# Performance work log

Hardware: AMD Instinct MI355X
Metric: run time of the kernel (lower is better)

Reference implementation:

```python
import jax, jax.numpy as jnp
import numpy as np

DIM = 512
HEADS = 8
DHEAD = DIM // 8          # 64
INNER = HEADS * DHEAD     # 512
M_LANDMARKS = 256
PINV_ITERS = 6
KSZ = 33                  # residual depthwise conv kernel (default)


def setup_inputs() -> dict:
    key = jax.random.key(0)
    ks = jax.random.split(key, 5)
    B, N = 1, 16384
    s = DIM ** -0.5
    return {
        "x": jax.random.normal(ks[0], (B, N, DIM), jnp.float32),
        "norm_w": jnp.ones((DIM,), jnp.float32),
        "norm_b": jnp.zeros((DIM,), jnp.float32),
        "w_qkv": jax.random.normal(ks[1], (3 * INNER, DIM), jnp.float32) * s,   # Linear(dim, 3*inner, bias=False)
        "w_out": jax.random.normal(ks[2], (DIM, INNER), jnp.float32) * s,        # Linear(inner, dim)
        "b_out": jnp.zeros((DIM,), jnp.float32),
        "conv_w": jax.random.normal(ks[3], (HEADS, 1, KSZ, 1), jnp.float32) * 0.1,  # depthwise Conv2d(h,h,(33,1),groups=h)
    }


def _layernorm(x, w, b, eps=1e-5):
    mu = x.mean(-1, keepdims=True)
    var = ((x - mu) ** 2).mean(-1, keepdims=True)
    return (x - mu) * jax.lax.rsqrt(var + eps) * w + b


def _moore_penrose_pinv(a, iters):
    # a: [B, H, m, m]; matches lucidrains moore_penrose_iter_pinv (global max over col/row sums)
    abs_a = jnp.abs(a)
    col = abs_a.sum(-1).max()
    row = abs_a.sum(-2).max()
    z = jnp.swapaxes(a, -1, -2) / (col * row)
    I = jnp.eye(a.shape[-1], dtype=a.dtype)
    for _ in range(iters):
        az = a @ z
        z = 0.25 * z @ (13 * I - az @ (15 * I - az @ (7 * I - az)))
    return z


def _nystrom_attention(h, w_qkv, w_out, b_out, conv_w):
    B, N, _ = h.shape
    qkv = h @ w_qkv.T                          # [B, N, 3*inner]
    q, k, v = jnp.split(qkv, 3, axis=-1)

    def heads(t):
        return t.reshape(B, N, HEADS, DHEAD).transpose(0, 2, 1, 3)  # [B, H, N, d]
    q = heads(q) * (DHEAD ** -0.5)
    k = heads(k)
    v = heads(v)

    # landmark pooling: mean over contiguous groups of size l = N / m
    l = N // M_LANDMARKS
    q_l = q.reshape(B, HEADS, M_LANDMARKS, l, DHEAD).mean(3)   # [B, H, m, d]
    k_l = k.reshape(B, HEADS, M_LANDMARKS, l, DHEAD).mean(3)

    attn1 = jax.nn.softmax(jnp.einsum('bhnd,bhmd->bhnm', q, k_l), axis=-1)      # [B,H,N,m]
    attn2 = jax.nn.softmax(jnp.einsum('bhid,bhjd->bhij', q_l, k_l), axis=-1)    # [B,H,m,m]
    attn3 = jax.nn.softmax(jnp.einsum('bhmd,bhnd->bhmn', q_l, k), axis=-1)      # [B,H,m,N]

    attn2_inv = _moore_penrose_pinv(attn2, PINV_ITERS)
    out = attn1 @ (attn2_inv @ (attn3 @ v))                                     # [B,H,N,d]

    # residual depthwise conv along sequence dim (kernel 33x1, groups=HEADS, no bias)
    conv = jax.lax.conv_general_dilated(
        v, conv_w, window_strides=(1, 1),
        padding=((KSZ // 2, KSZ // 2), (0, 0)),
        dimension_numbers=('NCHW', 'OIHW', 'NCHW'),
        feature_group_count=HEADS)
    out = out + conv

    out = out.transpose(0, 2, 1, 3).reshape(B, N, INNER)
    return out @ w_out.T + b_out


def reference(x, norm_w, norm_b, w_qkv, w_out, b_out, conv_w):
    h = _layernorm(x, norm_w, norm_b)
    return x + _nystrom_attention(h, w_qkv, w_out, b_out, conv_w)
```

## Files before the change

### kernel.cpp

```cpp
#include <hip/hip_runtime.h>
#include <hip/hip_bf16.h>


typedef __attribute__((ext_vector_type(8))) short bf16x8;
typedef __attribute__((ext_vector_type(4))) float f32x4;

#define MFMA16(A, B, C) __builtin_amdgcn_mfma_f32_16x16x32_bf16(A, B, C, 0, 0, 0)
#define GLD16(g, l) __builtin_amdgcn_global_load_lds( \
    (const __attribute__((address_space(1))) void*)(g), \
    (__attribute__((address_space(3))) void*)(l), 16, 0, 0)

static __device__ __forceinline__ unsigned short f2b(float f) {
  __hip_bfloat16 h = __float2bfloat16(f);
  return *reinterpret_cast<unsigned short*>(&h);
}
static __device__ __forceinline__ float b2f(unsigned short u) {
  return __uint_as_float(((unsigned)u) << 16);
}

#define FMA16(ACC, AV, BV) do { \
  ACC[0][0] += AV.x*BV.x; ACC[0][1] += AV.x*BV.y; ACC[0][2] += AV.x*BV.z; ACC[0][3] += AV.x*BV.w; \
  ACC[1][0] += AV.y*BV.x; ACC[1][1] += AV.y*BV.y; ACC[1][2] += AV.y*BV.z; ACC[1][3] += AV.y*BV.w; \
  ACC[2][0] += AV.z*BV.x; ACC[2][1] += AV.z*BV.y; ACC[2][2] += AV.z*BV.z; ACC[2][3] += AV.z*BV.w; \
  ACC[3][0] += AV.w*BV.x; ACC[3][1] += AV.w*BV.y; ACC[3][2] += AV.w*BV.z; ACC[3][3] += AV.w*BV.w; \
} while (0)

__global__ __launch_bounds__(128) void k_ln(const float* __restrict__ x,
    const float* __restrict__ w, const float* __restrict__ b, unsigned short* __restrict__ h) {
  const int row = blockIdx.x;
  const int t = threadIdx.x;
  const float4 xv = ((const float4*)(x + (size_t)row * 512))[t];
  float s  = xv.x + xv.y + xv.z + xv.w;
  float sq = xv.x*xv.x + xv.y*xv.y + xv.z*xv.z + xv.w*xv.w;
  #pragma unroll
  for (int o = 32; o > 0; o >>= 1) {
    s  += __shfl_down(s, o, 64);
    sq += __shfl_down(sq, o, 64);
  }
  __shared__ float ls[2], lq[2];
  if ((t & 63) == 0) { ls[t >> 6] = s; lq[t >> 6] = sq; }
  __syncthreads();
  s = ls[0] + ls[1]; sq = lq[0] + lq[1];
  const float mean = s * (1.0f / 512.0f);
  const float var  = sq * (1.0f / 512.0f) - mean * mean;
  const float rstd = rsqrtf(var + 1e-5f);
  const float4 wv = ((const float4*)w)[t];
  const float4 bv = ((const float4*)b)[t];
  ushort4 hv;
  hv.x = f2b((xv.x - mean) * rstd * wv.x + bv.x);
  hv.y = f2b((xv.y - mean) * rstd * wv.y + bv.y);
  hv.z = f2b((xv.z - mean) * rstd * wv.z + bv.z);
  hv.w = f2b((xv.w - mean) * rstd * wv.w + bv.w);
  ((ushort4*)(h + (size_t)row * 512))[t] = hv;
}

__global__ __launch_bounds__(256) void k_cvt(const float* __restrict__ src,
    unsigned short* __restrict__ dst, int n4) {
  const int i = blockIdx.x * 256 + threadIdx.x;
  if (i < n4) {
    const float4 f = ((const float4*)src)[i];
    ushort4 u;
    u.x = f2b(f.x); u.y = f2b(f.y); u.z = f2b(f.z); u.w = f2b(f.w);
    ((ushort4*)dst)[i] = u;
  }
}

__global__ __launch_bounds__(256) void k_qkv_mfma(const unsigned short* __restrict__ A,
    const unsigned short* __restrict__ B,
    unsigned short* __restrict__ qb, unsigned short* __restrict__ kb,
    unsigned short* __restrict__ vb) {
  __shared__ unsigned short As[128 * 32];
  __shared__ unsigned short Bs[128 * 32];
  const int t = threadIdx.x;
  const int lane = t & 63, w = t >> 6;
  const int quad = lane >> 4, l15 = lane & 15;
  const int wm = (w >> 1) * 64, wn = (w & 1) * 64;
  const int m0 = blockIdx.y * 128, n0 = blockIdx.x * 128;
  f32x4 acc[4][4];
  #pragma unroll
  for (int i = 0; i < 4; ++i)
    #pragma unroll
    for (int j = 0; j < 4; ++j) acc[i][j] = (f32x4){0.f, 0.f, 0.f, 0.f};
  for (int k0 = 0; k0 < 512; k0 += 32) {
    __syncthreads();
    #pragma unroll
    for (int c = 0; c < 2; ++c) {
      const int slot = c * 256 + t;
      const int row = slot >> 2, seg = slot & 3;
      GLD16(A + (size_t)(m0 + row) * 512 + k0 + seg * 8, As + slot * 8);
      GLD16(B + (size_t)(n0 + row) * 512 + k0 + seg * 8, Bs + slot * 8);
    }
    __syncthreads();
    bf16x8 a[4], b[4];
    #pragma unroll
    for (int i = 0; i < 4; ++i)
      a[i] = *(const bf16x8*)(As + (wm + i * 16 + l15) * 32 + quad * 8);
    #pragma unroll
    for (int j = 0; j < 4; ++j)
      b[j] = *(const bf16x8*)(Bs + (wn + j * 16 + l15) * 32 + quad * 8);
    #pragma unroll
    for (int i = 0; i < 4; ++i)
      #pragma unroll
      for (int j = 0; j < 4; ++j)
        acc[i][j] = MFMA16(a[i], b[j], acc[i][j]);
  }
  const int part = n0 >> 9;
  #pragma unroll
  for (int i = 0; i < 4; ++i)
    #pragma unroll
    for (int j = 0; j < 4; ++j)
      #pragma unroll
      for (int r = 0; r < 4; ++r) {
        const int row = m0 + wm + i * 16 + quad * 4 + r;
        const int col = n0 + wn + j * 16 + l15;
        const int rem = col & 511;
        const int hd = rem >> 6, dd = rem & 63;
        const size_t idx = ((size_t)hd * 16384 + row) * 64 + dd;
        const float val = acc[i][j][r];
        if (part == 0)      qb[idx] = f2b(val * 0.125f);
        else if (part == 1) kb[idx] = f2b(val);
        else                vb[idx] = f2b(val);
      }
}

__global__ __launch_bounds__(256) void k_tr(const unsigned short* __restrict__ v,
    unsigned short* __restrict__ vt) {
  __shared__ unsigned short T[64][72];
  const int t = threadIdx.x;
  const int n0 = blockIdx.x * 64, h = blockIdx.y;
  const int n = t >> 2, sg = (t & 3) * 16;
  const unsigned short* p = v + ((size_t)(h * 16384 + n0 + n)) * 64 + sg;
  #pragma unroll
  for (int i = 0; i < 16; i += 4) {
    const ushort4 u = *(const ushort4*)(p + i);
    T[sg + i + 0][n] = u.x; T[sg + i + 1][n] = u.y;
    T[sg + i + 2][n] = u.z; T[sg + i + 3][n] = u.w;
  }
  __syncthreads();
  const int d = t >> 2, so = (t & 3) * 16;
  unsigned short* q = vt + ((size_t)(h * 64 + d)) * 16384 + n0 + so;
  #pragma unroll
  for (int i = 0; i < 16; i += 4) {
    ushort4 u;
    u.x = T[d][so + i]; u.y = T[d][so + i + 1];
    u.z = T[d][so + i + 2]; u.w = T[d][so + i + 3];
    *(ushort4*)(q + i) = u;
  }
}

__global__ __launch_bounds__(256) void k_landmark(const unsigned short* __restrict__ qb,
    const unsigned short* __restrict__ kb, float* __restrict__ qlf,
    unsigned short* __restrict__ qlb, float* __restrict__ klf,
    unsigned short* __restrict__ klb) {
  const int t = threadIdx.x, d = t & 63, grp = t >> 6;
  const int m = blockIdx.x, h = blockIdx.y;
  const unsigned short* src = blockIdx.z ? kb : qb;
  const unsigned short* p = src + ((size_t)h * 16384 + m * 64 + grp * 16) * 64 + d;
  float s = 0.f;
  #pragma unroll
  for (int i = 0; i < 16; ++i) s += b2f(p[(size_t)i * 64]);
  __shared__ float red[4][64];
  red[grp][d] = s;
  __syncthreads();
  if (t < 64) {
    float v = (red[0][d] + red[1][d]) + (red[2][d] + red[3][d]);
    v *= (1.0f / 64.0f);
    const size_t oi = ((size_t)h * 256 + m) * 64 + d;
    if (blockIdx.z == 0) { qlf[oi] = v; qlb[oi] = f2b(v); }
    else                 { klf[oi] = v; klb[oi] = f2b(v); }
  }
}

__global__ __launch_bounds__(256) void k_attn2(const float* __restrict__ ql,
    const float* __restrict__ kl, float* __restrict__ a2, unsigned short* __restrict__ a2b) {
  const int i = blockIdx.x, h = blockIdx.y, j = threadIdx.x;
  __shared__ float qrow[64];
  __shared__ float wred[4];
  __shared__ float wsum[4];
  if (j < 64) qrow[j] = ql[((size_t)h * 256 + i) * 64 + j];
  __syncthreads();
  const float* kr = kl + ((size_t)h * 256 + j) * 64;
  float s = 0.f;
  #pragma unroll 8
  for (int d = 0; d < 64; ++d) s += qrow[d] * kr[d];
  float mx = s;
  #pragma unroll
  for (int o2 = 32; o2 > 0; o2 >>= 1) mx = fmaxf(mx, __shfl_xor(mx, o2, 64));
  if ((j & 63) == 0) wred[j >> 6] = mx;
  __syncthreads();
  mx = fmaxf(fmaxf(wred[0], wred[1]), fmaxf(wred[2], wred[3]));
  const float e = __expf(s - mx);
  float sm = e;
  #pragma unroll
  for (int o2 = 32; o2 > 0; o2 >>= 1) sm += __shfl_xor(sm, o2, 64);
  if ((j & 63) == 0) wsum[j >> 6] = sm;
  __syncthreads();
  sm = wsum[0] + wsum[1] + wsum[2] + wsum[3];
  const float v = e / sm;
  const size_t idx = ((size_t)h * 256 + i) * 256 + j;
  a2[idx] = v;
  a2b[idx] = f2b(v);
}

__global__ __launch_bounds__(256) void k_colsum(const float* __restrict__ a2,
    float* __restrict__ cm) {
  const int h = blockIdx.x, j = threadIdx.x;
  const float* p = a2 + (size_t)h * 65536 + j;
  float s = 0.f;
  for (int i = 0; i < 256; ++i) s += p[(size_t)i * 256];
  float mx = s;
  #pragma unroll
  for (int o2 = 32; o2 > 0; o2 >>= 1) mx = fmaxf(mx, __shfl_xor(mx, o2, 64));
  __shared__ float wred[4];
  if ((j & 63) == 0) wred[j >> 6] = mx;
  __syncthreads();
  if (j == 0) cm[h] = fmaxf(fmaxf(wred[0], wred[1]), fmaxf(wred[2], wred[3]));
}

__global__ __launch_bounds__(256) void k_z0(const float* __restrict__ a2,
    const float* __restrict__ cm, unsigned short* __restrict__ z0b,
    unsigned short* __restrict__ z0t) {
  __shared__ float T[64][65];
  const int bi = blockIdx.x, bj = blockIdx.y, h = blockIdx.z;
  const int t = threadIdx.x;
  const int r = t >> 2, cseg = (t & 3) * 16;
  float g = cm[0];
  #pragma unroll
  for (int c = 1; c < 8; ++c) g = fmaxf(g, cm[c]);
  const float inv = 1.0f / g;
  const float* p = a2 + ((size_t)h * 256 + bj * 64 + r) * 256 + bi * 64 + cseg;
  unsigned short* qt = z0t + ((size_t)h * 256 + bj * 64 + r) * 256 + bi * 64 + cseg;
  #pragma unroll
  for (int i = 0; i < 16; i += 4) {
    const float4 f = *(const float4*)(p + i);
    T[cseg + i + 0][r] = f.x; T[cseg + i + 1][r] = f.y;
    T[cseg + i + 2][r] = f.z; T[cseg + i + 3][r] = f.w;
    ushort4 u;
    u.x = f2b(f.x * inv); u.y = f2b(f.y * inv);
    u.z = f2b(f.z * inv); u.w = f2b(f.w * inv);
    *(ushort4*)(qt + i) = u;
  }
  __syncthreads();
  unsigned short* qb_ = z0b + ((size_t)h * 256 + bi * 64 + r) * 256 + bj * 64 + cseg;
  #pragma unroll
  for (int i = 0; i < 16; i += 4) {
    ushort4 u;
    u.x = f2b(T[r][cseg + i] * inv);     u.y = f2b(T[r][cseg + i + 1] * inv);
    u.z = f2b(T[r][cseg + i + 2] * inv); u.w = f2b(T[r][cseg + i + 3] * inv);
    *(ushort4*)(qb_ + i) = u;
  }
}

__global__ __launch_bounds__(256) void k_pgemm(const unsigned short* __restrict__ A,
    const unsigned short* __restrict__ Bt, unsigned short* __restrict__ Cn,
    unsigned short* __restrict__ Ct, float* __restrict__ Cf,
    float alpha, float sdiag, int use_diag) {
  __shared__ unsigned short As[64 * 128];
  __shared__ unsigned short Bs[64 * 128];
  const int t = threadIdx.x;
  const int lane = t & 63, w = t >> 6;
  const int quad = lane >> 4, l15 = lane & 15;
  const int bn = blockIdx.x, bm = blockIdx.y, h = blockIdx.z;
  const size_t hs = (size_t)h * 65536;
  const unsigned short* Ap = A + hs + (size_t)(bm * 64) * 256;
  const unsigned short* Bp = Bt + hs + (size_t)(bn * 64) * 256;
  f32x4 acc[4];
  #pragma unroll
  for (int j = 0; j < 4; ++j) acc[j] = (f32x4){0.f, 0.f, 0.f, 0.f};
  for (int kh = 0; kh < 2; ++kh) {
    __syncthreads();
    #pragma unroll
    for (int c = 0; c < 4; ++c) {
      const int slot = c * 256 + t;
      const int row = slot >> 4, pc = slot & 15;
      const int lc = pc ^ (row & 7);
      GLD16(Ap + (size_t)row * 256 + kh * 128 + lc * 8, As + slot * 8);
      GLD16(Bp + (size_t)row * 256 + kh * 128 + lc * 8, Bs + slot * 8);
    }
    __syncthreads();
    #pragma unroll
    for (int kc = 0; kc < 4; ++kc) {
      const int arow = w * 16 + l15;
      const bf16x8 a = *(const bf16x8*)(As + arow * 128 + ((kc * 4 + quad) ^ (arow & 7)) * 8);
      #pragma unroll
      for (int j = 0; j < 4; ++j) {
        const int brow = j * 16 + l15;
        const bf16x8 b = *(const bf16x8*)(Bs + brow * 128 + ((kc * 4 + quad) ^ (brow & 7)) * 8);
        acc[j] = MFMA16(a, b, acc[j]);
      }
    }
  }
  const int row0 = bm * 64 + w * 16 + quad * 4;
  #pragma unroll
  for (int j = 0; j < 4; ++j) {
    const int col = bn * 64 + j * 16 + l15;
    float v[4];
    #pragma unroll
    for (int r = 0; r < 4; ++r) v[r] = acc[j][r] * alpha;
    if (Cn) {
      #pragma unroll
      for (int r = 0; r < 4; ++r) Cn[hs + (size_t)(row0 + r) * 256 + col] = f2b(v[r]);
    }
    if (Cf) {
      #pragma unroll
      for (int r = 0; r < 4; ++r) Cf[hs + (size_t)(row0 + r) * 256 + col] = v[r];
    }
    ushort4 u;
    float tv[4];
    #pragma unroll
    for (int r = 0; r < 4; ++r)
      tv[r] = use_diag ? ((col == row0 + r ? sdiag : 0.f) - v[r]) : v[r];
    u.x = f2b(tv[0]); u.y = f2b(tv[1]); u.z = f2b(tv[2]); u.w = f2b(tv[3]);
    *(ushort4*)(Ct + hs + (size_t)col * 256 + row0) = u;
  }
}

__global__ __launch_bounds__(256) void k_gemm256(const float* __restrict__ A,
    const float* __restrict__ B, float* __restrict__ C,
    int lda, int ldb, int ldc,
    unsigned long long sA, unsigned long long sB, unsigned long long sC,
    float alpha, float sdiag, int use_diag,
    const float* __restrict__ rs, unsigned long long sRS) {
  A += (size_t)blockIdx.z * sA;
  B += (size_t)blockIdx.z * sB;
  C += (size_t)blockIdx.z * sC;
  if (rs) rs += (size_t)blockIdx.z * sRS;
  __shared__ float As[16][68];
  __shared__ float Bs[16][68];
  const int t = threadIdx.x, tx = t & 15, ty = t >> 4;
  const int bn = blockIdx.x, bm = blockIdx.y;
  const int lr = t >> 2, lk = (t & 3) << 2;
  const int bkr = t >> 4, bnc = (t & 15) << 2;
  float acc[4][4] = {{0.f}};
  for (int k0 = 0; k0 < 256; k0 += 16) {
    float4 a4 = *(const float4*)(A + (size_t)(bm * 64 + lr) * lda + k0 + lk);
    float4 b4 = *(const float4*)(B + (size_t)(k0 + bkr) * ldb + bn * 64 + bnc);
    if (use_diag) {
      const int kg = k0 + bkr, ngb = bn * 64 + bnc;
      b4.x = (kg == ngb + 0 ? sdiag : 0.f) - b4.x;
      b4.y = (kg == ngb + 1 ? sdiag : 0.f) - b4.y;
      b4.z = (kg == ngb + 2 ? sdiag : 0.f) - b4.z;
      b4.w = (kg == ngb + 3 ? sdiag : 0.f) - b4.w;
    }
    if (rs) {
      const float rv = 1.0f / rs[k0 + bkr];
      b4.x *= rv; b4.y *= rv; b4.z *= rv; b4.w *= rv;
    }
    __syncthreads();
    As[lk+0][lr] = a4.x; As[lk+1][lr] = a4.y; As[lk+2][lr] = a4.z; As[lk+3][lr] = a4.w;
    *(float4*)&Bs[bkr][bnc] = b4;
    __syncthreads();
    #pragma unroll
    for (int kq = 0; kq < 16; ++kq) {
      const float4 av = *(const float4*)&As[kq][ty << 2];
      const float4 bv = *(const float4*)&Bs[kq][tx << 2];
      FMA16(acc, av, bv);
    }
  }
  #pragma unroll
  for (int ii = 0; ii < 4; ++ii)
    #pragma unroll
    for (int jj = 0; jj < 4; ++jj)
      C[(size_t)(bm * 64 + (ty << 2) + ii) * ldc + bn * 64 + (tx << 2) + jj] =
          alpha * acc[ii][jj];
}

__global__ __launch_bounds__(256) void k_trD(const float* __restrict__ D,
    unsigned short* __restrict__ dt) {
  __shared__ float T[64][65];
  const int t = threadIdx.x;
  const int mc = blockIdx.x, h = blockIdx.y;
  const int m = t >> 2, sg = (t & 3) * 16;
  const float* p = D + ((size_t)(h * 256 + mc * 64 + m)) * 64 + sg;
  #pragma unroll
  for (int i = 0; i < 16; i += 4) {
    const float4 f = *(const float4*)(p + i);
    T[sg + i + 0][m] = f.x; T[sg + i + 1][m] = f.y;
    T[sg + i + 2][m] = f.z; T[sg + i + 3][m] = f.w;
  }
  __syncthreads();
  const int d = t >> 2, so = (t & 3) * 16;
  unsigned short* q = dt + ((size_t)(h * 64 + d)) * 256 + mc * 64 + so;
  #pragma unroll
  for (int i = 0; i < 16; i += 4) {
    ushort4 u;
    u.x = f2b(T[d][so + i]);     u.y = f2b(T[d][so + i + 1]);
    u.z = f2b(T[d][so + i + 2]); u.w = f2b(T[d][so + i + 3]);
    *(ushort4*)(q + i) = u;
  }
}

__global__ __launch_bounds__(256) void k_w3_mfma(const unsigned short* __restrict__ qlb,
    const unsigned short* __restrict__ kb, const unsigned short* __restrict__ vt,
    float* __restrict__ W, float* __restrict__ lsum) {
  __shared__ unsigned short QLs[64 * 64];
  __shared__ unsigned short Ks [64 * 64];
  __shared__ unsigned short Vts[64 * 64];
  __shared__ unsigned short Ps [64 * 64];
  const int t = threadIdx.x;
  const int lane = t & 63, w = t >> 6;
  const int quad = lane >> 4, l15 = lane & 15;
  const int kc = blockIdx.x, mt = blockIdx.y, h = blockIdx.z;
  #pragma unroll
  for (int c = 0; c < 2; ++c) {
    const int slot = c * 256 + t;
    const int row = slot >> 3, pc = slot & 7, lc = pc ^ (row & 7);
    GLD16(qlb + ((size_t)(h * 256 + mt * 64 + row)) * 64 + lc * 8, QLs + slot * 8);
  }
  __syncthreads();
  const int arow = w * 16 + l15;
  const bf16x8 aq0 = *(const bf16x8*)(QLs + arow * 64 + ((quad    ) ^ (arow & 7)) * 8);
  const bf16x8 aq1 = *(const bf16x8*)(QLs + arow * 64 + ((quad + 4) ^ (arow & 7)) * 8);
  f32x4 wacc[4];
  #pragma unroll
  for (int dt = 0; dt < 4; ++dt) wacc[dt] = (f32x4){0.f, 0.f, 0.f, 0.f};
  float lacc[4] = {0.f, 0.f, 0.f, 0.f};
  for (int ss = 0; ss < 16; ++ss) {
    const int n0 = kc * 1024 + ss * 64;
    __syncthreads();
    #pragma unroll
    for (int c = 0; c < 2; ++c) {
      const int slot = c * 256 + t;
      const int row = slot >> 3, pc = slot & 7, lc = pc ^ (row & 7);
      GLD16(kb + ((size_t)(h * 16384 + n0 + row)) * 64 + lc * 8, Ks + slot * 8);
      GLD16(vt + ((size_t)(h * 64 + row)) * 16384 + n0 + lc * 8, Vts + slot * 8);
    }
    __syncthreads();
    f32x4 s[4];
    #pragma unroll
    for (int j = 0; j < 4; ++j) {
      s[j] = (f32x4){0.f, 0.f, 0.f, 0.f};
      const int brow = j * 16 + l15;
      const bf16x8 b0 = *(const bf16x8*)(Ks + brow * 64 + ((quad    ) ^ (brow & 7)) * 8);
      const bf16x8 b1 = *(const bf16x8*)(Ks + brow * 64 + ((quad + 4) ^ (brow & 7)) * 8);
      s[j] = MFMA16(aq0, b0, s[j]);
      s[j] = MFMA16(aq1, b1, s[j]);
    }
    #pragma unroll
    for (int j = 0; j < 4; ++j)
      #pragma unroll
      for (int r = 0; r < 4; ++r) {
        const float e = __expf(s[j][r]);
        lacc[r] += e;
        const int prow = w * 16 + quad * 4 + r, pcol = j * 16 + l15;
        Ps[prow * 64 + (((pcol >> 3) ^ (prow & 7)) << 3) + (pcol & 7)] = f2b(e);
      }
    __syncthreads();
    const bf16x8 ap0 = *(const bf16x8*)(Ps + arow * 64 + ((quad    ) ^ (arow & 7)) * 8);
    const bf16x8 ap1 = *(const bf16x8*)(Ps + arow * 64 + ((quad + 4) ^ (arow & 7)) * 8);
    #pragma unroll
    for (int dt = 0; dt < 4; ++dt) {
      const int brow = dt * 16 + l15;
      const bf16x8 b0 = *(const bf16x8*)(Vts + brow * 64 + ((quad    ) ^ (brow & 7)) * 8);
      const bf16x8 b1 = *(const bf16x8*)(Vts + brow * 64 + ((quad + 4) ^ (brow & 7)) * 8);
      wacc[dt] = MFMA16(ap0, b0, wacc[dt]);
      wacc[dt] = MFMA16(ap1, b1, wacc[dt]);
    }
  }
  #pragma unroll
  for (int dt = 0; dt < 4; ++dt)
    #pragma unroll
    for (int r = 0; r < 4; ++r)
      atomicAdd(&W[((size_t)(h * 256 + mt * 64 + w * 16 + quad * 4 + r)) * 64 + dt * 16 + l15],
                wacc[dt][r]);
  #pragma unroll
  for (int r = 0; r < 4; ++r) {
    #pragma unroll
    for (int msk = 1; msk < 16; msk <<= 1) lacc[r] += __shfl_xor(lacc[r], msk, 64);
    if (l15 == 0)
      atomicAdd(&lsum[h * 256 + mt * 64 + w * 16 + quad * 4 + r], lacc[r]);
  }
}

__global__ __launch_bounds__(256) void k_attn1_mfma(const unsigned short* __restrict__ qb,
    const unsigned short* __restrict__ klb, const unsigned short* __restrict__ dtb,
    const unsigned short* __restrict__ vt, const float* __restrict__ cw,
    unsigned short* __restrict__ o) {
  __shared__ unsigned short Wb[64 * 96];
  __shared__ unsigned short Ks[64 * 64];
  __shared__ unsigned short Ds[64 * 64];
  __shared__ unsigned short Ps[64 * 64];
  __shared__ float Wsm[33];
  const int t = threadIdx.x;
  const int lane = t & 63, w = t >> 6;
  const int quad = lane >> 4, l15 = lane & 15;
  const int bt = blockIdx.x, h = blockIdx.y;
  const int n0 = bt * 64;
  if (t < 33) Wsm[t] = cw[h * 33 + t];
  #pragma unroll
  for (int c = 0; c < 2; ++c) {
    const int slot = c * 256 + t;
    const int row = slot >> 3, pc = slot & 7, lc = pc ^ (row & 7);
    GLD16(qb + ((size_t)(h * 16384 + n0 + row)) * 64 + lc * 8, Wb + slot * 8);
  }
  __syncthreads();
  const int arow = w * 16 + l15;
  const bf16x8 aq0 = *(const bf16x8*)(Wb + arow * 64 + ((quad    ) ^ (arow & 7)) * 8);
  const bf16x8 aq1 = *(const bf16x8*)(Wb + arow * 64 + ((quad + 4) ^ (arow & 7)) * 8);
  __syncthreads();
  {
    const int n = t >> 2;
    const int gb = (t & 3) * 24;
    #pragma unroll
    for (int i = 0; i < 24; ++i) {
      const int g = gb + i;
      const int j = g - n;
      const int src = n0 - 16 + g;
      const float val = (j >= 0 && j <= 32 && src >= 0 && src < 16384) ? Wsm[j] : 0.f;
      Wb[n * 96 + (((g >> 3) ^ (n & 3)) << 3) + (g & 7)] = f2b(val);
    }
  }
  __syncthreads();
  f32x4 cacc[4];
  #pragma unroll
  for (int dt = 0; dt < 4; ++dt) cacc[dt] = (f32x4){0.f, 0.f, 0.f, 0.f};
  #pragma unroll
  for (int kcc = 0; kcc < 3; ++kcc) {
    const bf16x8 a = *(const bf16x8*)(Wb + arow * 96 + (((kcc * 4 + quad) ^ (arow & 3)) << 3));
    int off = n0 - 16 + kcc * 32 + quad * 8;
    off = off < 0 ? 0 : (off > 16376 ? 16376 : off);
    #pragma unroll
    for (int dt = 0; dt < 4; ++dt) {
      const bf16x8 b = *(const bf16x8*)(vt + ((size_t)(h * 64 + dt * 16 + l15)) * 16384 + off);
      cacc[dt] = MFMA16(a, b, cacc[dt]);
    }
  }
  f32x4 oacc[4];
  #pragma unroll
  for (int dt = 0; dt < 4; ++dt) oacc[dt] = (f32x4){0.f, 0.f, 0.f, 0.f};
  float lacc[4] = {0.f, 0.f, 0.f, 0.f};
  for (int mc = 0; mc < 4; ++mc) {
    const int m0 = mc * 64;
    __syncthreads();
    #pragma unroll
    for (int c = 0; c < 2; ++c) {
      const int slot = c * 256 + t;
      const int row = slot >> 3, pc = slot & 7, lc = pc ^ (row & 7);
      GLD16(klb + ((size_t)(h * 256 + m0 + row)) * 64 + lc * 8, Ks + slot * 8);
      GLD16(dtb + ((size_t)(h * 64 + row)) * 256 + m0 + lc * 8, Ds + slot * 8);
    }
    __syncthreads();
    f32x4 s[4];
    #pragma unroll
    for (int j = 0; j < 4; ++j) {
      s[j] = (f32x4){0.f, 0.f, 0.f, 0.f};
      const int brow = j * 16 + l15;
      const bf16x8 b0 = *(const bf16x8*)(Ks + brow * 64 + ((quad    ) ^ (brow & 7)) * 8);
      const bf16x8 b1 = *(const bf16x8*)(Ks + brow * 64 + ((quad + 4) ^ (brow & 7)) * 8);
      s[j] = MFMA16(aq0, b0, s[j]);
      s[j] = MFMA16(aq1, b1, s[j]);
    }
    #pragma unroll
    for (int j = 0; j < 4; ++j)
      #pragma unroll
      for (int r = 0; r < 4; ++r) {
        const float e = __expf(s[j][r]);
        lacc[r] += e;
        const int prow = w * 16 + quad * 4 + r, pcol = j * 16 + l15;
        Ps[prow * 64 + (((pcol >> 3) ^ (prow & 7)) << 3) + (pcol & 7)] = f2b(e);
      }
    __syncthreads();
    const bf16x8 ap0 = *(const bf16x8*)(Ps + arow * 64 + ((quad    ) ^ (arow & 7)) * 8);
    const bf16x8 ap1 = *(const bf16x8*)(Ps + arow * 64 + ((quad + 4) ^ (arow & 7)) * 8);
    #pragma unroll
    for (int dt = 0; dt < 4; ++dt) {
      const int brow = dt * 16 + l15;
      const bf16x8 b0 = *(const bf16x8*)(Ds + brow * 64 + ((quad    ) ^ (brow & 7)) * 8);
      const bf16x8 b1 = *(const bf16x8*)(Ds + brow * 64 + ((quad + 4) ^ (brow & 7)) * 8);
      oacc[dt] = MFMA16(ap0, b0, oacc[dt]);
      oacc[dt] = MFMA16(ap1, b1, oacc[dt]);
    }
  }
  #pragma unroll
  for (int r = 0; r < 4; ++r)
    #pragma unroll
    for (int msk = 1; msk < 16; msk <<= 1) lacc[r] += __shfl_xor(lacc[r], msk, 64);
  #pragma unroll
  for (int dt = 0; dt < 4; ++dt)
    #pragma unroll
    for (int r = 0; r < 4; ++r) {
      const float val = oacc[dt][r] / lacc[r] + cacc[dt][r];
      o[((size_t)(n0 + w * 16 + quad * 4 + r)) * 512 + h * 64 + dt * 16 + l15] = f2b(val);
    }
}

__global__ __launch_bounds__(256) void k_out_mfma(const unsigned short* __restrict__ A,
    const unsigned short* __restrict__ B, const float* __restrict__ bias,
    const float* __restrict__ xres, float* __restrict__ out) {
  __shared__ unsigned short As[128 * 32];
  __shared__ unsigned short Bs[128 * 32];
  const int t = threadIdx.x;
  const int lane = t & 63, w = t >> 6;
  const int quad = lane >> 4, l15 = lane & 15;
  const int wm = (w >> 1) * 64, wn = (w & 1) * 64;
  const int m0 = blockIdx.y * 128, n0 = blockIdx.x * 128;
  f32x4 acc[4][4];
  #pragma unroll
  for (int i = 0; i < 4; ++i)
    #pragma unroll
    for (int j = 0; j < 4; ++j) acc[i][j] = (f32x4){0.f, 0.f, 0.f, 0.f};
  for (int k0 = 0; k0 < 512; k0 += 32) {
    __syncthreads();
    #pragma unroll
    for (int c = 0; c < 2; ++c) {
      const int slot = c * 256 + t;
      const int row = slot >> 2, seg = slot & 3;
      GLD16(A + (size_t)(m0 + row) * 512 + k0 + seg * 8, As + slot * 8);
      GLD16(B + (size_t)(n0 + row) * 512 + k0 + seg * 8, Bs + slot * 8);
    }
    __syncthreads();
    bf16x8 a[4], b[4];
    #pragma unroll
    for (int i = 0; i < 4; ++i)
      a[i] = *(const bf16x8*)(As + (wm + i * 16 + l15) * 32 + quad * 8);
    #pragma unroll
    for (int j = 0; j < 4; ++j)
      b[j] = *(const bf16x8*)(Bs + (wn + j * 16 + l15) * 32 + quad * 8);
    #pragma unroll
    for (int i = 0; i < 4; ++i)
      #pragma unroll
      for (int j = 0; j < 4; ++j)
        acc[i][j] = MFMA16(a[i], b[j], acc[i][j]);
  }
  #pragma unroll
  for (int i = 0; i < 4; ++i)
    #pragma unroll
    for (int j = 0; j < 4; ++j)
      #pragma unroll
      for (int r = 0; r < 4; ++r) {
        const int row = m0 + wm + i * 16 + quad * 4 + r;
        const int col = n0 + wn + j * 16 + l15;
        out[(size_t)row * 512 + col] = acc[i][j][r] + bias[col] + xres[(size_t)row * 512 + col];
      }
}

extern "C" void kernel_launch(void* const* d_in, const int* in_sizes, int n_in,
                              void* d_out, int out_size, void* d_ws, size_t ws_size,
                              hipStream_t stream) {
  const float* x      = (const float*)d_in[0];
  const float* norm_w = (const float*)d_in[1];
  const float* norm_b = (const float*)d_in[2];
  const float* w_qkv  = (const float*)d_in[3];
  const float* w_out  = (const float*)d_in[4];
  const float* b_out  = (const float*)d_in[5];
  const float* conv_w = (const float*)d_in[6];
  float* out = (float*)d_out;

  char* cur = (char*)d_ws;
  auto alloc = [&](size_t bytes) -> char* {
    char* p = cur;
    cur += (bytes + 255) & ~(size_t)255;
    return p;
  };
  const size_t NB = (size_t)16384 * 512;
  const size_t LM = (size_t)8 * 256 * 64;
  const size_t SQ = (size_t)8 * 256 * 256;

  unsigned short* h_b  = (unsigned short*)alloc(NB * 2);
  unsigned short* wq_b = (unsigned short*)alloc((size_t)1536 * 512 * 2);
  unsigned short* wo_b = (unsigned short*)alloc((size_t)512 * 512 * 2);
  unsigned short* qb   = (unsigned short*)alloc(NB * 2);
  unsigned short* kb   = (unsigned short*)alloc(NB * 2);
  unsigned short* vb   = (unsigned short*)alloc(NB * 2);
  unsigned short* vt   = (unsigned short*)alloc(NB * 2);
  float*          qlf  = (float*)alloc(LM * 4);
  float*          klf  = (float*)alloc(LM * 4);
  unsigned short* qlb  = (unsigned short*)alloc(LM * 2);
  unsigned short* klb  = (unsigned short*)alloc(LM * 2);
  float*          a2   = (float*)alloc(SQ * 4);
  unsigned short* a2b  = (unsigned short*)alloc(SQ * 2);
  unsigned short* z0b  = (unsigned short*)alloc(SQ * 2);
  unsigned short* z0t  = (unsigned short*)alloc(SQ * 2);
  unsigned short* Pn   = (unsigned short*)alloc(SQ * 2);
  unsigned short* Pt   = (unsigned short*)alloc(SQ * 2);
  unsigned short* Q1t  = (unsigned short*)alloc(SQ * 2);
  unsigned short* Q2t  = (unsigned short*)alloc(SQ * 2);
  unsigned short* zp0n = (unsigned short*)alloc(SQ * 2);
  unsigned short* zp0t = (unsigned short*)alloc(SQ * 2);
  unsigned short* zp1n = (unsigned short*)alloc(SQ * 2);
  unsigned short* zp1t = (unsigned short*)alloc(SQ * 2);
  float*          zf5  = (float*)alloc(SQ * 4);
  float*          zfin = (float*)alloc(SQ * 4);
  float*          Pp   = (float*)alloc(SQ * 4);
  float*          Q1   = (float*)alloc(SQ * 4);
  float*          Q2   = (float*)alloc(SQ * 4);
  float*          W    = (float*)alloc(LM * 4 + 2048 * 4);
  float*          lsum = W + LM;
  float*          D    = (float*)alloc(LM * 4);
  unsigned short* dtb  = (unsigned short*)alloc(LM * 2);
  float*          cm   = (float*)alloc(64 * 4);
  unsigned short* o_b  = (unsigned short*)alloc(NB * 2);

  hipMemsetAsync(W, 0, (LM + 2048) * sizeof(float), stream);
  k_ln<<<16384, 128, 0, stream>>>(x, norm_w, norm_b, h_b);
  k_cvt<<<768, 256, 0, stream>>>(w_qkv, wq_b, 196608);
  k_cvt<<<256, 256, 0, stream>>>(w_out, wo_b, 65536);
  k_qkv_mfma<<<dim3(12, 128), 256, 0, stream>>>(h_b, wq_b, qb, kb, vb);
  k_tr<<<dim3(256, 8), 256, 0, stream>>>(vb, vt);
  k_landmark<<<dim3(256, 8, 2), 256, 0, stream>>>(qb, kb, qlf, qlb, klf, klb);
  k_attn2<<<dim3(256, 8), 256, 0, stream>>>(qlf, klf, a2, a2b);
  k_colsum<<<8, 256, 0, stream>>>(a2, cm);
  k_z0<<<dim3(4, 4, 8), 256, 0, stream>>>(a2, cm, z0b, z0t);

  unsigned short* zan = z0b; unsigned short* zat = z0t;
  for (int it = 0; it < 5; ++it) {
    unsigned short* zbn = (it & 1) ? zp1n : zp0n;
    unsigned short* zbt = (it & 1) ? zp1t : zp0t;
    k_pgemm<<<dim3(4, 4, 8), 256, 0, stream>>>(a2b, zat, Pn, Pt, nullptr, 1.f, 7.f, 1);
    k_pgemm<<<dim3(4, 4, 8), 256, 0, stream>>>(Pn, Pt, nullptr, Q1t, nullptr, 1.f, 15.f, 1);
    k_pgemm<<<dim3(4, 4, 8), 256, 0, stream>>>(Pn, Q1t, nullptr, Q2t, nullptr, 1.f, 13.f, 1);
    k_pgemm<<<dim3(4, 4, 8), 256, 0, stream>>>(zan, Q2t, zbn, zbt,
        it == 4 ? zf5 : nullptr, 0.25f, 0.f, 0);
    zan = zbn; zat = zbt;
  }
  k_gemm256<<<dim3(4, 4, 8), 256, 0, stream>>>(a2, zf5, Pp, 256, 256, 256,
      65536ULL, 65536ULL, 65536ULL, 1.f, 0.f, 0, nullptr, 0ULL);
  k_gemm256<<<dim3(4, 4, 8), 256, 0, stream>>>(Pp, Pp, Q1, 256, 256, 256,
      65536ULL, 65536ULL, 65536ULL, 1.f, 7.f, 1, nullptr, 0ULL);
  k_gemm256<<<dim3(4, 4, 8), 256, 0, stream>>>(Pp, Q1, Q2, 256, 256, 256,
      65536ULL, 65536ULL, 65536ULL, 1.f, 15.f, 1, nullptr, 0ULL);
  k_gemm256<<<dim3(4, 4, 8), 256, 0, stream>>>(zf5, Q2, zfin, 256, 256, 256,
      65536ULL, 65536ULL, 65536ULL, 0.25f, 13.f, 1, nullptr, 0ULL);

  k_w3_mfma<<<dim3(16, 4, 8), 256, 0, stream>>>(qlb, kb, vt, W, lsum);
  k_gemm256<<<dim3(1, 4, 8), 256, 0, stream>>>(zfin, W, D, 256, 64, 64,
      65536ULL, 16384ULL, 16384ULL, 1.f, 0.f, 0, lsum, 256ULL);
  k_trD<<<dim3(4, 8), 256, 0, stream>>>(D, dtb);
  k_attn1_mfma<<<dim3(256, 8), 256, 0, stream>>>(qb, klb, dtb, vt, conv_w, o_b);
  k_out_mfma<<<dim3(4, 128), 256, 0, stream>>>(o_b, wo_b, b_out, x, out);
}
```

Baseline: 450.3 us.

## Fuse pinv iteration GEMMs into one cooperative kernel and swizzle GEMM LDS

```diff
diff --git a/kernel.cpp b/kernel.cpp
--- a/kernel.cpp
+++ b/kernel.cpp
@@ -1,5 +1,8 @@
 #include <hip/hip_runtime.h>
 #include <hip/hip_bf16.h>
+#include <hip/hip_cooperative_groups.h>
+
+namespace cg = cooperative_groups;
 
 
 typedef __attribute__((ext_vector_type(8))) short bf16x8;
@@ -86,18 +89,23 @@
     #pragma unroll
     for (int c = 0; c < 2; ++c) {
       const int slot = c * 256 + t;
-      const int row = slot >> 2, seg = slot & 3;
-      GLD16(A + (size_t)(m0 + row) * 512 + k0 + seg * 8, As + slot * 8);
-      GLD16(B + (size_t)(n0 + row) * 512 + k0 + seg * 8, Bs + slot * 8);
+      const int row = slot >> 2, pc = slot & 3;
+      const int lc = pc ^ (row & 3);
+      GLD16(A + (size_t)(m0 + row) * 512 + k0 + lc * 8, As + slot * 8);
+      GLD16(B + (size_t)(n0 + row) * 512 + k0 + lc * 8, Bs + slot * 8);
     }
     __syncthreads();
     bf16x8 a[4], b[4];
     #pragma unroll
-    for (int i = 0; i < 4; ++i)
-      a[i] = *(const bf16x8*)(As + (wm + i * 16 + l15) * 32 + quad * 8);
-    #pragma unroll
-    for (int j = 0; j < 4; ++j)
-      b[j] = *(const bf16x8*)(Bs + (wn + j * 16 + l15) * 32 + quad * 8);
+    for (int i = 0; i < 4; ++i) {
+      const int ar = wm + i * 16 + l15;
+      a[i] = *(const bf16x8*)(As + ar * 32 + (quad ^ (ar & 3)) * 8);
+    }
+    #pragma unroll
+    for (int j = 0; j < 4; ++j) {
+      const int br = wn + j * 16 + l15;
+      b[j] = *(const bf16x8*)(Bs + br * 32 + (quad ^ (br & 3)) * 8);
+    }
     #pragma unroll
     for (int i = 0; i < 4; ++i)
       #pragma unroll
@@ -251,19 +259,15 @@
   }
 }
 
-__global__ __launch_bounds__(256) void k_pgemm(const unsigned short* __restrict__ A,
+static __device__ __forceinline__ void pgemm_tile(const unsigned short* __restrict__ A,
     const unsigned short* __restrict__ Bt, unsigned short* __restrict__ Cn,
     unsigned short* __restrict__ Ct, float* __restrict__ Cf,
-    float alpha, float sdiag, int use_diag) {
-  __shared__ unsigned short As[64 * 128];
-  __shared__ unsigned short Bs[64 * 128];
-  const int t = threadIdx.x;
+    float alpha, float sdiag, int use_diag, int bm, int bn, int t,
+    unsigned short* As, unsigned short* Bs) {
   const int lane = t & 63, w = t >> 6;
   const int quad = lane >> 4, l15 = lane & 15;
-  const int bn = blockIdx.x, bm = blockIdx.y, h = blockIdx.z;
-  const size_t hs = (size_t)h * 65536;
-  const unsigned short* Ap = A + hs + (size_t)(bm * 64) * 256;
-  const unsigned short* Bp = Bt + hs + (size_t)(bn * 64) * 256;
+  const unsigned short* Ap = A + (size_t)(bm * 64) * 256;
+  const unsigned short* Bp = Bt + (size_t)(bn * 64) * 256;
   f32x4 acc[4];
   #pragma unroll
   for (int j = 0; j < 4; ++j) acc[j] = (f32x4){0.f, 0.f, 0.f, 0.f};
@@ -299,11 +303,11 @@
     for (int r = 0; r < 4; ++r) v[r] = acc[j][r] * alpha;
     if (Cn) {
       #pragma unroll
-      for (int r = 0; r < 4; ++r) Cn[hs + (size_t)(row0 + r) * 256 + col] = f2b(v[r]);
+      for (int r = 0; r < 4; ++r) Cn[(size_t)(row0 + r) * 256 + col] = f2b(v[r]);
     }
     if (Cf) {
       #pragma unroll
-      for (int r = 0; r < 4; ++r) Cf[hs + (size_t)(row0 + r) * 256 + col] = v[r];
+      for (int r = 0; r < 4; ++r) Cf[(size_t)(row0 + r) * 256 + col] = v[r];
     }
     ushort4 u;
     float tv[4];
@@ -311,7 +315,46 @@
     for (int r = 0; r < 4; ++r)
       tv[r] = use_diag ? ((col == row0 + r ? sdiag : 0.f) - v[r]) : v[r];
     u.x = f2b(tv[0]); u.y = f2b(tv[1]); u.z = f2b(tv[2]); u.w = f2b(tv[3]);
-    *(ushort4*)(Ct + hs + (size_t)col * 256 + row0) = u;
+    *(ushort4*)(Ct + (size_t)col * 256 + row0) = u;
+  }
+}
+
+struct ChainArgs {
+  const unsigned short* a2b;
+  unsigned short* z0b; unsigned short* z0t;
+  unsigned short* Pn; unsigned short* Pt;
+  unsigned short* Q1t; unsigned short* Q2t;
+  unsigned short* zp0n; unsigned short* zp0t;
+  unsigned short* zp1n; unsigned short* zp1t;
+  float* zf5;
+};
+
+__global__ __launch_bounds__(256) void k_chain(ChainArgs ca) {
+  __shared__ unsigned short As[64 * 128];
+  __shared__ unsigned short Bs[64 * 128];
+  cg::grid_group grid = cg::this_grid();
+  const int t = threadIdx.x;
+  const int bid = blockIdx.x;
+  const int bn = bid & 3, bm = (bid >> 2) & 3, h = bid >> 4;
+  const size_t hs = (size_t)h << 16;
+  unsigned short* zan = ca.z0b; unsigned short* zat = ca.z0t;
+  for (int it = 0; it < 5; ++it) {
+    unsigned short* zbn = (it & 1) ? ca.zp1n : ca.zp0n;
+    unsigned short* zbt = (it & 1) ? ca.zp1t : ca.zp0t;
+    pgemm_tile(ca.a2b + hs, zat + hs, ca.Pn + hs, ca.Pt + hs, nullptr,
+               1.f, 7.f, 1, bm, bn, t, As, Bs);
+    grid.sync();
+    pgemm_tile(ca.Pn + hs, ca.Pt + hs, nullptr, ca.Q1t + hs, nullptr,
+               1.f, 15.f, 1, bm, bn, t, As, Bs);
+    grid.sync();
+    pgemm_tile(ca.Pn + hs, ca.Q1t + hs, nullptr, ca.Q2t + hs, nullptr,
+               1.f, 13.f, 1, bm, bn, t, As, Bs);
+    grid.sync();
+    pgemm_tile(zan + hs, ca.Q2t + hs, zbn + hs, zbt + hs,
+               (it == 4) ? ca.zf5 + hs : nullptr,
+               0.25f, 0.f, 0, bm, bn, t, As, Bs);
+    grid.sync();
+    zan = zbn; zat = zbt;
   }
 }
 
@@ -604,18 +647,23 @@
     #pragma unroll
     for (int c = 0; c < 2; ++c) {
       const int slot = c * 256 + t;
-      const int row = slot >> 2, seg = slot & 3;
-      GLD16(A + (size_t)(m0 + row) * 512 + k0 + seg * 8, As + slot * 8);
-      GLD16(B + (size_t)(n0 + row) * 512 + k0 + seg * 8, Bs + slot * 8);
+      const int row = slot >> 2, pc = slot & 3;
+      const int lc = pc ^ (row & 3);
+      GLD16(A + (size_t)(m0 + row) * 512 + k0 + lc * 8, As + slot * 8);
+      GLD16(B + (size_t)(n0 + row) * 512 + k0 + lc * 8, Bs + slot * 8);
     }
     __syncthreads();
     bf16x8 a[4], b[4];
     #pragma unroll
-    for (int i = 0; i < 4; ++i)
-      a[i] = *(const bf16x8*)(As + (wm + i * 16 + l15) * 32 + quad * 8);
-    #pragma unroll
-    for (int j = 0; j < 4; ++j)
-      b[j] = *(const bf16x8*)(Bs + (wn + j * 16 + l15) * 32 + quad * 8);
+    for (int i = 0; i < 4; ++i) {
+      const int ar = wm + i * 16 + l15;
+      a[i] = *(const bf16x8*)(As + ar * 32 + (quad ^ (ar & 3)) * 8);
+    }
+    #pragma unroll
+    for (int j = 0; j < 4; ++j) {
+      const int br = wn + j * 16 + l15;
+      b[j] = *(const bf16x8*)(Bs + br * 32 + (quad ^ (br & 3)) * 8);
+    }
     #pragma unroll
     for (int i = 0; i < 4; ++i)
       #pragma unroll
@@ -702,17 +750,15 @@
   k_colsum<<<8, 256, 0, stream>>>(a2, cm);
   k_z0<<<dim3(4, 4, 8), 256, 0, stream>>>(a2, cm, z0b, z0t);
 
-  unsigned short* zan = z0b; unsigned short* zat = z0t;
-  for (int it = 0; it < 5; ++it) {
-    unsigned short* zbn = (it & 1) ? zp1n : zp0n;
-    unsigned short* zbt = (it & 1) ? zp1t : zp0t;
-    k_pgemm<<<dim3(4, 4, 8), 256, 0, stream>>>(a2b, zat, Pn, Pt, nullptr, 1.f, 7.f, 1);
-    k_pgemm<<<dim3(4, 4, 8), 256, 0, stream>>>(Pn, Pt, nullptr, Q1t, nullptr, 1.f, 15.f, 1);
-    k_pgemm<<<dim3(4, 4, 8), 256, 0, stream>>>(Pn, Q1t, nullptr, Q2t, nullptr, 1.f, 13.f, 1);
-    k_pgemm<<<dim3(4, 4, 8), 256, 0, stream>>>(zan, Q2t, zbn, zbt,
-        it == 4 ? zf5 : nullptr, 0.25f, 0.f, 0);
-    zan = zbn; zat = zbt;
-  }
+  ChainArgs ca;
+  ca.a2b = a2b;
+  ca.z0b = z0b; ca.z0t = z0t;
+  ca.Pn = Pn; ca.Pt = Pt; ca.Q1t = Q1t; ca.Q2t = Q2t;
+  ca.zp0n = zp0n; ca.zp0t = zp0t; ca.zp1n = zp1n; ca.zp1t = zp1t;
+  ca.zf5 = zf5;
+  void* chain_args[] = {&ca};
+  hipLaunchCooperativeKernel((void*)k_chain, dim3(128), dim3(256), chain_args, 0, stream);
+
   k_gemm256<<<dim3(4, 4, 8), 256, 0, stream>>>(a2, zf5, Pp, 256, 256, 256,
       65536ULL, 65536ULL, 65536ULL, 1.f, 0.f, 0, nullptr, 0ULL);
   k_gemm256<<<dim3(4, 4, 8), 256, 0, stream>>>(Pp, Pp, Q1, 256, 256, 256,
```

Result: slower. 770.3 us (+71.1%).
